# Performance work log

Measured on AMD Instinct MI355X. Metric: run time of the kernel, lower is better.

## Reference

```python
import jax, jax.numpy as jnp
import numpy as np

FACTOR = 2  # upsample factor from init_kwargs


def _make_kernel_2d(kernel_1d):
    # outer product -> 2D separable FIR kernel, normalized to sum 1,
    # then scaled by factor**2 (gain compensation for zero-insertion upsampling)
    k = kernel_1d[None, :] * kernel_1d[:, None]
    k = k / jnp.sum(k)
    return k * (FACTOR ** 2)


def setup_inputs() -> dict:
    key = jax.random.key(0)
    k1, k2 = jax.random.split(key)
    x = jax.random.normal(k1, (8, 64, 256, 256), dtype=jnp.float32)
    # canonical StyleGAN FIR taps [1,3,3,1]
    kernel_1d = jnp.asarray([1.0, 3.0, 3.0, 1.0], dtype=jnp.float32)
    return {"x": x, "kernel_1d": kernel_1d}


def reference(x, kernel_1d):
    # upfirdn2d(x, k, up=factor, down=1, pad=(pad0, pad1))
    k2d = _make_kernel_2d(kernel_1d)            # [kh, kw]
    kh = k2d.shape[0]
    p = kh - FACTOR
    pad0 = (p + 1) // 2 + FACTOR - 1
    pad1 = p // 2

    # upfirdn uses true convolution (kernel flipped relative to correlation)
    kf = jnp.flip(k2d, (0, 1))
    C = x.shape[1]
    # depthwise filter, OIHW with I=1, same FIR taps for every channel
    w = jnp.broadcast_to(kf[None, None, :, :], (C, 1, kh, kh)).astype(x.dtype)

    # lhs_dilation fuses the zero-insertion upsample; padding fuses the pad step.
    # out spatial: FACTOR*(H-1)+1 + pad0 + pad1 - kh + 1 == FACTOR*H
    out = jax.lax.conv_general_dilated(
        x, w,
        window_strides=(1, 1),
        padding=((pad0, pad1), (pad0, pad1)),
        lhs_dilation=(FACTOR, FACTOR),
        dimension_numbers=("NCHW", "OIHW", "NCHW"),
        feature_group_count=C,
    )
    return out  # [B, C, FACTOR*H, FACTOR*W]
```

## Files before the change

### kernel.cpp

```cpp
#include <hip/hip_runtime.h>


#define IN_H 256
#define IN_W 256
#define OUT_H 511
#define OUT_W 511
#define N_BC (8 * 64)
#define QY 32
#define STRIPS (IN_H / QY)

__global__ __launch_bounds__(256) void Upsample_64948495450678_kernel(
    const float* __restrict__ x,
    const float* __restrict__ k1d,
    float* __restrict__ out)
{
    const int qx  = threadIdx.x;
    const int blk = blockIdx.x;
    const int bc  = blk >> 3;
    const int y0  = (blk & (STRIPS - 1)) * QY;

    const float k0 = k1d[0], k1 = k1d[1], k2 = k1d[2], k3 = k1d[3];
    const float inv = 2.0f / (k0 + k1 + k2 + k3);
    const float k0i = k0 * inv, k1i = k1 * inv, k2i = k2 * inv, k3i = k3 * inv;

    const float* __restrict__ xp = x + (size_t)bc * (IN_H * IN_W);
    const float* pin = xp + (size_t)y0 * IN_W + qx;
    float* pout = out + (size_t)bc * ((size_t)OUT_H * OUT_W)
                      + (size_t)(2 * y0) * OUT_W + 2 * qx;

    float a, am;
    if (y0 == 0) {
        a = 0.0f; am = 0.0f;
    } else {
        a  = pin[-IN_W];
        am = qx ? pin[-IN_W - 1] : 0.0f;
    }

    #pragma unroll 4
    for (int i = 0; i < QY; ++i) {
        const float b  = pin[0];
        const float bm = qx ? pin[-1] : 0.0f;

        const float Hto = k2i * am + k0i * a;
        const float Hte = k3i * am + k1i * a;
        const float Hbo = k2i * bm + k0i * b;
        const float Hbe = k3i * bm + k1i * b;

        if (y0 + i > 0) {
            if (qx > 0) pout[-OUT_W - 1] = k2i * Hto + k0i * Hbo;
            pout[-OUT_W] = k2i * Hte + k0i * Hbe;
        }
        if (qx > 0) pout[-1] = k3i * Hto + k1i * Hbo;
        pout[0] = k3i * Hte + k1i * Hbe;

        a = b; am = bm;
        pin  += IN_W;
        pout += 2 * OUT_W;
    }
}

extern "C" void kernel_launch(void* const* d_in, const int* in_sizes, int n_in,
                              void* d_out, int out_size, void* d_ws, size_t ws_size,
                              hipStream_t stream) {
    const float* x   = (const float*)d_in[0];
    const float* k1d = (const float*)d_in[1];
    float* out = (float*)d_out;

    dim3 block(256, 1, 1);
    dim3 grid(N_BC * STRIPS, 1, 1);
    Upsample_64948495450678_kernel<<<grid, block, 0, stream>>>(x, k1d, out);
}
```

Measured before the change: 693.0 us.

## Remap threads to contiguous output columns for coalesced stores, split strip rows

Each thread now produces contiguous output columns (tx, tx+128, ...) instead of two adjacent output pixels, so warp stores are unit-stride rather than stride-2. Input reads use a parity-dependent tap pair, and the 32-row strip is split between two 128-thread halves of the block. The aim is fully coalesced writes on the write-dominated output. In exchange each thread does more redundant input loads per row and there is a boundary column special case.

```diff
diff --git a/kernel.cpp b/kernel.cpp
--- a/kernel.cpp
+++ b/kernel.cpp
@@ -8,52 +8,71 @@
 #define N_BC (8 * 64)
 #define QY 32
 #define STRIPS (IN_H / QY)
+#define HR (QY / 2)
 
 __global__ __launch_bounds__(256) void Upsample_64948495450678_kernel(
     const float* __restrict__ x,
     const float* __restrict__ k1d,
     float* __restrict__ out)
 {
-    const int qx  = threadIdx.x;
-    const int blk = blockIdx.x;
-    const int bc  = blk >> 3;
-    const int y0  = (blk & (STRIPS - 1)) * QY;
+    const int t  = threadIdx.x;
+    const int tx = t & 127;
+    const int ty = t >> 7;
+    const int bc = blockIdx.x >> 3;
+    const int r0 = (blockIdx.x & (STRIPS - 1)) * QY + ty * HR;
 
     const float k0 = k1d[0], k1 = k1d[1], k2 = k1d[2], k3 = k1d[3];
     const float inv = 2.0f / (k0 + k1 + k2 + k3);
-    const float k0i = k0 * inv, k1i = k1 * inv, k2i = k2 * inv, k3i = k3 * inv;
+    const float k0i = k0*inv, k1i = k1*inv, k2i = k2*inv, k3i = k3*inv;
 
-    const float* __restrict__ xp = x + (size_t)bc * (IN_H * IN_W);
-    const float* pin = xp + (size_t)y0 * IN_W + qx;
-    float* pout = out + (size_t)bc * ((size_t)OUT_H * OUT_W)
-                      + (size_t)(2 * y0) * OUT_W + 2 * qx;
+    const int   p  = tx & 1;
+    const float wA = p ? k2i : k3i;
+    const float wB = p ? k0i : k1i;
+    const int   q0 = (tx >> 1) + p;
+    const bool  s3 = (tx < 127);
 
-    float a, am;
-    if (y0 == 0) {
-        a = 0.0f; am = 0.0f;
+    const float* __restrict__ xim = x + (size_t)bc * (IN_H * IN_W);
+    const float* pin = xim + (size_t)r0 * IN_W;
+
+    auto hrow = [&](const float* __restrict__ prow, float H[4]) {
+        const float xa0 = (q0 > 0) ? prow[q0 - 1] : 0.0f;
+        H[0] = wA * xa0            + wB * prow[q0];
+        H[1] = wA * prow[q0 + 63]  + wB * prow[q0 + 64];
+        H[2] = wA * prow[q0 + 127] + wB * prow[q0 + 128];
+        if (s3)
+            H[3] = wA * prow[q0 + 191] + wB * prow[q0 + 192];
+        else
+            H[3] = 0.0f;
+    };
+
+    float Hp[4];
+    if (r0 == 0) {
+        Hp[0] = Hp[1] = Hp[2] = Hp[3] = 0.0f;
     } else {
-        a  = pin[-IN_W];
-        am = qx ? pin[-IN_W - 1] : 0.0f;
+        hrow(pin - IN_W, Hp);
     }
 
+    float* pout = out + (size_t)bc * ((size_t)OUT_H * OUT_W)
+                      + (size_t)(2 * r0) * OUT_W + tx;
+
     #pragma unroll 4
-    for (int i = 0; i < QY; ++i) {
-        const float b  = pin[0];
-        const float bm = qx ? pin[-1] : 0.0f;
+    for (int i = 0; i < HR; ++i) {
+        float H[4];
+        hrow(pin, H);
 
-        const float Hto = k2i * am + k0i * a;
-        const float Hte = k3i * am + k1i * a;
-        const float Hbo = k2i * bm + k0i * b;
-        const float Hbe = k3i * bm + k1i * b;
+        if (r0 + i > 0) {
+            float* po = pout - OUT_W;
+            po[0]   = k2i * Hp[0] + k0i * H[0];
+            po[128] = k2i * Hp[1] + k0i * H[1];
+            po[256] = k2i * Hp[2] + k0i * H[2];
+            if (s3) po[384] = k2i * Hp[3] + k0i * H[3];
+        }
+        pout[0]   = k3i * Hp[0] + k1i * H[0];
+        pout[128] = k3i * Hp[1] + k1i * H[1];
+        pout[256] = k3i * Hp[2] + k1i * H[2];
+        if (s3) pout[384] = k3i * Hp[3] + k1i * H[3];
 
-        if (y0 + i > 0) {
-            if (qx > 0) pout[-OUT_W - 1] = k2i * Hto + k0i * Hbo;
-            pout[-OUT_W] = k2i * Hte + k0i * Hbe;
-        }
-        if (qx > 0) pout[-1] = k3i * Hto + k1i * Hbo;
-        pout[0] = k3i * Hte + k1i * Hbe;
-
-        a = b; am = bm;
+        Hp[0] = H[0]; Hp[1] = H[1]; Hp[2] = H[2]; Hp[3] = H[3];
         pin  += IN_W;
         pout += 2 * OUT_W;
     }
```

Result: faster. 671.6 us (-3.1%).
